# Performance work log

Measured on AMD Instinct MI355X. Metric: run time of the kernel, lower is better.

The kernel has to match this reference:

```python
import jax, jax.numpy as jnp
import numpy as np

B, T, H, LATENT, P = 64, 256, 1024, 256, 128


def _lstm_layer(x, h0, c0, Wih, Whh, bih, bhh):
    """PyTorch-convention single-direction LSTM layer.
    x: (B,T,Din); returns hidden sequence (B,T,H). Gate order: i,f,g,o."""
    # Precompute the input contribution for all timesteps in one big GEMM.
    xg = jnp.einsum('btd,gd->btg', x, Wih) + bih + bhh  # (B,T,4H)

    def step(carry, xg_t):
        h, c = carry
        gates = xg_t + h @ Whh.T  # (B,4H)
        i, f, g, o = jnp.split(gates, 4, axis=-1)
        c = jax.nn.sigmoid(f) * c + jax.nn.sigmoid(i) * jnp.tanh(g)
        h = jax.nn.sigmoid(o) * jnp.tanh(c)
        return (h, c), h

    (_, _), hs = jax.lax.scan(step, (h0, c0), jnp.swapaxes(xg, 0, 1))
    return jnp.swapaxes(hs, 0, 1)  # (B,T,H)


def setup_inputs() -> dict:
    key = jax.random.key(0)
    ks = jax.random.split(key, 8)
    s = lambda fan_in: 1.0 / np.sqrt(fan_in)
    return {
        'z': jax.random.normal(ks[0], (B, LATENT), jnp.float32),
        'target_seq': jax.random.uniform(ks[1], (B, T, P), jnp.float32),
        'fc_init_w': jax.random.normal(ks[2], (H, LATENT), jnp.float32) * s(LATENT),
        'fc_init_b': jnp.zeros((H,), jnp.float32),
        'start_token': jax.random.normal(ks[3], (1, 1, P), jnp.float32) * 0.1,
        'W_ih_l0': jax.random.normal(ks[4], (4 * H, P), jnp.float32) * s(P),
        'W_hh_l0': jax.random.normal(ks[5], (4 * H, H), jnp.float32) * s(H),
        'b_ih_l0': jnp.zeros((4 * H,), jnp.float32),
        'b_hh_l0': jnp.zeros((4 * H,), jnp.float32),
        'W_ih_l1': jax.random.normal(ks[6], (4 * H, H), jnp.float32) * s(H),
        'W_hh_l1': jax.random.normal(ks[7], (4 * H, H), jnp.float32) * s(H),
        'b_ih_l1': jnp.zeros((4 * H,), jnp.float32),
        'b_hh_l1': jnp.zeros((4 * H,), jnp.float32),
        'out_w': jax.random.normal(jax.random.fold_in(key, 99), (P, H), jnp.float32) * s(H),
        'out_b': jnp.zeros((P,), jnp.float32),
    }


def reference(z, target_seq, fc_init_w, fc_init_b, start_token,
              W_ih_l0, W_hh_l0, b_ih_l0, b_hh_l0,
              W_ih_l1, W_hh_l1, b_ih_l1, b_hh_l1,
              out_w, out_b):
    # h0 = fc_init(z), shared across both LSTM layers (repeat over num_layers).
    h0 = z @ fc_init_w.T + fc_init_b  # (B,H)
    c0 = jnp.zeros_like(h0)
    # Full teacher forcing (teacher_forcing_ratio=1.0): input at step t is
    # target_seq[:, t-1]; step 0 uses the learned start token. Dropout is in
    # eval mode (identity).
    x_in = jnp.concatenate(
        [jnp.broadcast_to(start_token, (z.shape[0], 1, start_token.shape[-1])),
         target_seq[:, :-1, :]], axis=1)  # (B,T,P)
    h1 = _lstm_layer(x_in, h0, c0, W_ih_l0, W_hh_l0, b_ih_l0, b_hh_l0)
    h2 = _lstm_layer(h1, h0, c0, W_ih_l1, W_hh_l1, b_ih_l1, b_hh_l1)
    return jax.nn.sigmoid(jnp.einsum('bth,ph->btp', h2, out_w) + out_b)  # (B,T,P)
```

## Files before the change

### kernel.cpp

```cpp
#include <hip/hip_runtime.h>
#include <hip/hip_bf16.h>
#include <stdint.h>

typedef __attribute__((ext_vector_type(8))) short short8;
typedef __attribute__((ext_vector_type(4))) float floatx4;

#define B_ 64
#define T_ 256
#define H_ 1024
#define LATENT_ 256
#define P_ 128
#define BH_ (B_ * H_)
#define MFMA_(a, b, c) __builtin_amdgcn_mfma_f32_16x16x32_bf16(a, b, c, 0, 0, 0)
#define PBI(n, row) (((n) + 4 * (row)) & 31)

#define PBUF_OFF 0
#define WHH_OFF  65536
#define WIH0_OFF 131072
#define LDS_TOTAL 139264

#define SLOTS 258
#define CIDX(lay, slot) (((size_t)(lay) * SLOTS + (slot)) * 256)
#define RIDX(lay, slot) (((size_t)(lay) * SLOTS + (slot)) * 128)
#define CNTW (2 * SLOTS * 256)
#define RDYW (2 * SLOTS * 128)


__device__ __forceinline__ float sigmoidf_(float x) {
    return 1.0f / (1.0f + __expf(-x));
}
__device__ __forceinline__ float tanh_fast(float x) {
    float e = __expf(2.0f * x);
    return 1.0f - 2.0f / (e + 1.0f);
}

__global__ __launch_bounds__(256) void cvt_f2b(
    const float* __restrict__ src, __hip_bfloat16* __restrict__ dst, int n)
{
    int i = (blockIdx.x * 256 + threadIdx.x) * 4;
    if (i < n) {
        float4 v = *(const float4*)(src + i);
        dst[i + 0] = __float2bfloat16(v.x);
        dst[i + 1] = __float2bfloat16(v.y);
        dst[i + 2] = __float2bfloat16(v.z);
        dst[i + 3] = __float2bfloat16(v.w);
    }
}

__global__ __launch_bounds__(256) void h0_kernel(
    const float* __restrict__ z,
    const float* __restrict__ fw,
    const float* __restrict__ fb,
    __hip_bfloat16* __restrict__ h1dst,
    __hip_bfloat16* __restrict__ h2dst,
    unsigned* __restrict__ cnt,
    unsigned* __restrict__ rdy)
{
    int idx = blockIdx.x * 256 + threadIdx.x;
    for (int i = idx; i < CNTW; i += 65536) cnt[i] = 0u;
    for (int i = idx; i < RDYW; i += 65536) {
        int slot = (i >> 7) % SLOTS;
        rdy[i] = (slot == 0) ? 1u : 0u;
    }
    int b = idx >> 10, j = idx & 1023;
    const float* zp = z + b * LATENT_;
    const float* wp = fw + j * LATENT_;
    float acc = fb[j];
    for (int k = 0; k < LATENT_; k += 4) {
        float4 zv = *(const float4*)(zp + k);
        float4 wv = *(const float4*)(wp + k);
        acc += zv.x * wv.x + zv.y * wv.y + zv.z * wv.z + zv.w * wv.w;
    }
    __hip_bfloat16 hb = __float2bfloat16(acc);
    int off = ((j >> 3) * 64 + b) * 8 + (j & 7);
    h1dst[off] = hb;
    h2dst[off] = hb;
}

struct PParams {
    const __hip_bfloat16 *tseqb, *stokb;
    const __hip_bfloat16 *Wih0b, *Whh0b, *Wih1b, *Whh1b, *owb;
    const float *bih0, *bhh0, *bih1, *bhh1, *ob;
    __hip_bfloat16 *h1seq;
    __hip_bfloat16 *h2seq;
    float* out;
    unsigned* cnt;
    unsigned* rdy;
};

__global__ __launch_bounds__(512, 2) void lstm_persistent(PParams p)
{
    extern __shared__ char dynlds[];
    float (*pbuf)[64][32] = (float (*)[64][32])(dynlds + PBUF_OFF);
    short8* whh8 = (short8*)(dynlds + WHH_OFF);
    short8* wx8  = (short8*)(dynlds + WIH0_OFF);

    const int tid  = threadIdx.x;
    const int bid  = blockIdx.x;
    const int wv   = tid >> 6;
    const int l    = tid & 63;
    const int l15  = l & 15;
    const int quad = l >> 4;
    const int ks   = quad * 8;
    const bool isL1 = bid < 128;
    const int colbase = (isL1 ? bid : bid - 128) * 8;
    const int hblk = colbase >> 3;
    const int r0l  = (l15 >> 3) * 8 + (l15 & 7);
    const int row0 = ((l15 >> 3)    ) * H_ + colbase + (l15 & 7);
    const int row1 = ((l15 >> 3) + 2) * H_ + colbase + (l15 & 7);

    auto h1slot = [&](int t) { return p.h1seq + (size_t)(t + 1) * BH_; };
    auto h2slot = [&](int t) { return p.h2seq + (size_t)(t + 1) * BH_; };

    auto wspin = [&](int lay, int slot) {
        if (l == 0) {
            const unsigned* rf = p.rdy + RIDX(lay, slot) + wv * 16;
            while (__hip_atomic_load(rf, __ATOMIC_RELAXED,
                                     __HIP_MEMORY_SCOPE_AGENT) == 0u)
                __builtin_amdgcn_s_sleep(2);
        }
        asm volatile("" ::: "memory");
    };

    {
        const short* Wh = (const short*)(isL1 ? p.Whh1b : p.Whh0b);
        for (int i = tid; i < 32 * 128; i += 512) {
            int r = i >> 7, kc = i & 127;
            int grow = (r >> 3) * H_ + colbase + (r & 7);
            whh8[r * 128 + (kc ^ (r & 7))] =
                *(const short8*)(Wh + (size_t)grow * H_ + kc * 8);
        }
        if (!isL1) {
            const short* Wx = (const short*)p.Wih0b;
            for (int i = tid; i < 32 * 16; i += 512) {
                int r = i >> 4, kc = i & 15;
                int grow = (r >> 3) * H_ + colbase + (r & 7);
                wx8[r * 16 + (kc ^ (r & 7))] =
                    *(const short8*)(Wx + (size_t)grow * P_ + kc * 8);
            }
        }
    }
    __syncthreads();

    const int cm  = tid >> 3;
    const int c0  = tid & 7;
    const int cj0 = colbase + c0;
    const float* bi = isL1 ? p.bih1 : p.bih0;
    const float* bh = isL1 ? p.bhh1 : p.bhh0;
    float bs[4];
#pragma unroll
    for (int g = 0; g < 4; ++g)
        bs[g] = bi[g * H_ + cj0] + bh[g * H_ + cj0];
    float creg = 0.0f;

    const int lay = isL1 ? 1 : 0;

    for (int phase = 0; phase <= T_; ++phase) {
        const bool doGemm = isL1 ? (phase >= 1) : (phase < T_);
        const int t = isL1 ? phase - 1 : phase;
        if (!doGemm) continue;

        floatx4 acc[8] = {};
        if (isL1) {
            wspin(1, phase - 1);
            const short* A2 = (const short*)h2slot(t - 1);
            short8 af2[16];
#pragma unroll
            for (int c = 0; c < 4; ++c)
#pragma unroll
                for (int mt = 0; mt < 4; ++mt) {
                    int kR = wv * 16 + c * 4 + quad;
                    af2[c * 4 + mt] = *(const short8*)(A2 +
                        ((long)(kR * 64 + mt * 16 + l15) << 3));
                }
            wspin(0, phase);
            const short* A1 = (const short*)h1slot(t);
            short8 af1[16];
#pragma unroll
            for (int c = 0; c < 4; ++c)
#pragma unroll
                for (int mt = 0; mt < 4; ++mt) {
                    int kR = wv * 16 + c * 4 + quad;
                    af1[c * 4 + mt] = *(const short8*)(A1 +
                        ((long)(kR * 64 + mt * 16 + l15) << 3));
                }
#pragma unroll
            for (int c = 0; c < 4; ++c) {
                int kR = wv * 16 + c * 4 + quad;
                short8 b0 = whh8[r0l * 128 + (kR ^ (r0l & 7))];
                short8 b1 = whh8[(r0l + 16) * 128 + (kR ^ (r0l & 7))];
#pragma unroll
                for (int mt = 0; mt < 4; ++mt) {
                    acc[2 * mt]     = MFMA_(af2[c * 4 + mt], b0, acc[2 * mt]);
                    acc[2 * mt + 1] = MFMA_(af2[c * 4 + mt], b1, acc[2 * mt + 1]);
                }
            }
            const short* w0 = (const short*)p.Wih1b + (long)row0 * H_;
            const short* w1 = (const short*)p.Wih1b + (long)row1 * H_;
#pragma unroll
            for (int c = 0; c < 4; ++c) {
                int kR = wv * 16 + c * 4 + quad;
                short8 b0 = *(const short8*)(w0 + kR * 8);
                short8 b1 = *(const short8*)(w1 + kR * 8);
#pragma unroll
                for (int mt = 0; mt < 4; ++mt) {
                    acc[2 * mt]     = MFMA_(af1[c * 4 + mt], b0, acc[2 * mt]);
                    acc[2 * mt + 1] = MFMA_(af1[c * 4 + mt], b1, acc[2 * mt + 1]);
                }
            }
        } else {
            const short* Ax; long xstr;
            if (t == 0) { Ax = (const short*)p.stokb; xstr = 0; }
            else { Ax = (const short*)p.tseqb + (long)(t - 1) * P_; xstr = (long)T_ * P_; }
            short8 xf[4];
            if (wv < 4) {
#pragma unroll
                for (int mt = 0; mt < 4; ++mt)
                    xf[mt] = *(const short8*)(Ax + (long)(mt * 16 + l15) * xstr + wv * 32 + ks);
            }
            wspin(0, phase);
            const short* Ah = (const short*)h1slot(t - 1);
            short8 af[16];
#pragma unroll
            for (int c = 0; c < 4; ++c)
#pragma unroll
                for (int mt = 0; mt < 4; ++mt) {
                    int kR = wv * 16 + c * 4 + quad;
                    af[c * 4 + mt] = *(const short8*)(Ah +
                        ((long)(kR * 64 + mt * 16 + l15) << 3));
                }
            if (wv < 4) {
                int kcx = wv * 4 + quad;
                short8 b0 = wx8[r0l * 16 + (kcx ^ (r0l & 7))];
                short8 b1 = wx8[(r0l + 16) * 16 + (kcx ^ (r0l & 7))];
#pragma unroll
                for (int mt = 0; mt < 4; ++mt) {
                    acc[2 * mt]     = MFMA_(xf[mt], b0, acc[2 * mt]);
                    acc[2 * mt + 1] = MFMA_(xf[mt], b1, acc[2 * mt + 1]);
                }
            }
#pragma unroll
            for (int c = 0; c < 4; ++c) {
                int kR = wv * 16 + c * 4 + quad;
                short8 b0 = whh8[r0l * 128 + (kR ^ (r0l & 7))];
                short8 b1 = whh8[(r0l + 16) * 128 + (kR ^ (r0l & 7))];
#pragma unroll
                for (int mt = 0; mt < 4; ++mt) {
                    acc[2 * mt]     = MFMA_(af[c * 4 + mt], b0, acc[2 * mt]);
                    acc[2 * mt + 1] = MFMA_(af[c * 4 + mt], b1, acc[2 * mt + 1]);
                }
            }
        }
#pragma unroll
        for (int mt = 0; mt < 4; ++mt)
#pragma unroll
            for (int nt = 0; nt < 2; ++nt)
#pragma unroll
                for (int r = 0; r < 4; ++r) {
                    int row = mt * 16 + quad * 4 + r;
                    pbuf[wv][row][PBI(nt * 16 + l15, row)] = acc[2 * mt + nt][r];
                }
        __syncthreads();

        {
            float v[4];
#pragma unroll
            for (int g = 0; g < 4; ++g) v[g] = bs[g];
#pragma unroll
            for (int w2 = 0; w2 < 8; ++w2)
#pragma unroll
                for (int g = 0; g < 4; ++g)
                    v[g] += pbuf[w2][cm][PBI(8 * g + c0, cm)];
            float cn = sigmoidf_(v[1]) * creg + sigmoidf_(v[0]) * tanh_fast(v[2]);
            float hv = sigmoidf_(v[3]) * tanh_fast(cn);
            creg = cn;
            __hip_bfloat16* hdst = isL1 ? h2slot(t) : h1slot(t);
            __hip_bfloat16 hb = __float2bfloat16(hv);
            unsigned short hu = *(unsigned short*)&hb;
            __hip_atomic_store((unsigned short*)hdst + hblk * 512 + tid, hu,
                               __ATOMIC_RELAXED, __HIP_MEMORY_SCOPE_AGENT);
        }

        __syncthreads();
        if (tid == 0) {
            __hip_atomic_fetch_add(p.cnt + CIDX(lay, t + 1) + (hblk >> 3) * 16,
                                   1u, __ATOMIC_RELAXED, __HIP_MEMORY_SCOPE_AGENT);
            if (bid == 128 || bid == 0) {
                unsigned* cb = p.cnt + CIDX(lay, t + 1);
                for (;;) {
                    unsigned ok = 1;
#pragma unroll
                    for (int i2 = 0; i2 < 16; ++i2)
                        ok &= (__hip_atomic_load(cb + i2 * 16, __ATOMIC_RELAXED,
                                                 __HIP_MEMORY_SCOPE_AGENT) >= 8u);
                    if (ok) break;
                    __builtin_amdgcn_s_sleep(1);
                }
                asm volatile("" ::: "memory");
                unsigned* rb = p.rdy + RIDX(lay, t + 1);
#pragma unroll
                for (int w = 0; w < 8; ++w)
                    __hip_atomic_store(rb + w * 16, 1u,
                                       __ATOMIC_RELAXED, __HIP_MEMORY_SCOPE_AGENT);
            }
        }
        __syncthreads();
    }

    {
        const int t = bid;
        wspin(1, t + 1);
        __syncthreads();

        const int nh = wv >> 1, kh = wv & 1;
        const short* A  = (const short*)h2slot(t);
        const short* Wb = (const short*)p.owb;
        floatx4 oacc[8] = {};
        for (int c = 0; c < 16; ++c) {
            int kk = kh * 512 + c * 32 + ks;
            short8 b0 = *(const short8*)(Wb + (long)(nh * 32 + l15) * H_ + kk);
            short8 b1 = *(const short8*)(Wb + (long)(nh * 32 + 16 + l15) * H_ + kk);
#pragma unroll
            for (int mt = 0; mt < 4; ++mt) {
                short8 a = *(const short8*)(A +
                    ((long)((kh * 64 + c * 4 + quad) * 64 + mt * 16 + l15) << 3));
                oacc[2 * mt]     = MFMA_(a, b0, oacc[2 * mt]);
                oacc[2 * mt + 1] = MFMA_(a, b1, oacc[2 * mt + 1]);
            }
        }
#pragma unroll
        for (int mt = 0; mt < 4; ++mt)
#pragma unroll
            for (int nt = 0; nt < 2; ++nt)
#pragma unroll
                for (int r = 0; r < 4; ++r) {
                    int row = mt * 16 + quad * 4 + r;
                    pbuf[wv][row][PBI(nt * 16 + l15, row)] = oacc[2 * mt + nt][r];
                }
        __syncthreads();
        for (int i = tid; i < 64 * 128; i += 512) {
            int m = i >> 7, pp2 = i & 127;
            int nh2 = pp2 >> 5, pc = pp2 & 31;
            float v = pbuf[2 * nh2][m][PBI(pc, m)] + pbuf[2 * nh2 + 1][m][PBI(pc, m)]
                    + p.ob[pp2];
            p.out[(long)m * (T_ * P_) + (long)t * P_ + pp2] = sigmoidf_(v);
        }
    }
}

extern "C" void kernel_launch(void* const* d_in, const int* in_sizes, int n_in,
                              void* d_out, int out_size, void* d_ws, size_t ws_size,
                              hipStream_t stream) {
    const float* z    = (const float*)d_in[0];
    const float* tseq = (const float*)d_in[1];
    const float* fw   = (const float*)d_in[2];
    const float* fb   = (const float*)d_in[3];
    const float* stok = (const float*)d_in[4];
    const float* Wih0 = (const float*)d_in[5];
    const float* Whh0 = (const float*)d_in[6];
    const float* bih0 = (const float*)d_in[7];
    const float* bhh0 = (const float*)d_in[8];
    const float* Wih1 = (const float*)d_in[9];
    const float* Whh1 = (const float*)d_in[10];
    const float* bih1 = (const float*)d_in[11];
    const float* bhh1 = (const float*)d_in[12];
    const float* ow   = (const float*)d_in[13];
    const float* ob   = (const float*)d_in[14];
    float* out = (float*)d_out;

    const size_t FULLH = (size_t)(T_ + 1) * BH_ * 2;
    char* ws = (char*)d_ws;
    size_t off = 0;
    __hip_bfloat16* Wih0b = (__hip_bfloat16*)(ws + off); off += (size_t)4 * H_ * P_ * 2;
    __hip_bfloat16* Whh0b = (__hip_bfloat16*)(ws + off); off += (size_t)4 * H_ * H_ * 2;
    __hip_bfloat16* Wih1b = (__hip_bfloat16*)(ws + off); off += (size_t)4 * H_ * H_ * 2;
    __hip_bfloat16* Whh1b = (__hip_bfloat16*)(ws + off); off += (size_t)4 * H_ * H_ * 2;
    __hip_bfloat16* owb   = (__hip_bfloat16*)(ws + off); off += (size_t)P_ * H_ * 2;
    __hip_bfloat16* tseqb = (__hip_bfloat16*)(ws + off); off += (size_t)B_ * T_ * P_ * 2;
    __hip_bfloat16* stokb = (__hip_bfloat16*)(ws + off); off += 256;
    __hip_bfloat16* h1seq = (__hip_bfloat16*)(ws + off); off += FULLH;
    __hip_bfloat16* h2seq = (__hip_bfloat16*)(ws + off); off += FULLH;
    unsigned* cnt         = (unsigned*)(ws + off);       off += (size_t)CNTW * 4;
    unsigned* rdy         = (unsigned*)(ws + off);       off += (size_t)RDYW * 4;

    auto cvt = [&](const float* s, __hip_bfloat16* d, int n) {
        hipLaunchKernelGGL(cvt_f2b, dim3((n / 4 + 255) / 256), dim3(256), 0, stream, s, d, n);
    };
    cvt(Wih0, Wih0b, 4 * H_ * P_);
    cvt(Whh0, Whh0b, 4 * H_ * H_);
    cvt(Wih1, Wih1b, 4 * H_ * H_);
    cvt(Whh1, Whh1b, 4 * H_ * H_);
    cvt(ow,   owb,   P_ * H_);
    cvt(tseq, tseqb, B_ * T_ * P_);
    cvt(stok, stokb, P_);

    hipLaunchKernelGGL(h0_kernel, dim3(256), dim3(256), 0, stream,
                       z, fw, fb, h1seq, h2seq, cnt, rdy);

    PParams pp;
    pp.tseqb = tseqb; pp.stokb = stokb;
    pp.Wih0b = Wih0b; pp.Whh0b = Whh0b; pp.Wih1b = Wih1b; pp.Whh1b = Whh1b;
    pp.owb = owb;
    pp.bih0 = bih0; pp.bhh0 = bhh0; pp.bih1 = bih1; pp.bhh1 = bhh1; pp.ob = ob;
    pp.h1seq = h1seq; pp.h2seq = h2seq;
    pp.out = out;
    pp.cnt = cnt; pp.rdy = rdy;

    hipFuncSetAttribute((const void*)lstm_persistent,
                        hipFuncAttributeMaxDynamicSharedMemorySize, LDS_TOTAL);
    void* args[] = { &pp };
    hipLaunchCooperativeKernel((void*)lstm_persistent, dim3(256), dim3(512),
                               args, LDS_TOTAL, stream);
}
```

Baseline: 1.922 ms.

## Replace two-level counter/ready-flag barrier with per-group counters polled directly

Drops the aggregator blocks that waited on all per-step counters and then set ready flags. Each block now increments one of 8 group counters per layer and step, and consumers poll only the group counter covering the hidden-state slice their wave needs, waiting for 16 arrivals. This removes one hop of cross-block signalling and the trailing __syncthreads from the recurrent critical path. In exchange each wave waits only on its own slice, so correctness relies on the wave-to-group mapping matching the data each wave reads.

New measurement: 2.628 ms. +36.8%, slower.

```diff
diff --git a/kernel.cpp b/kernel.cpp
--- a/kernel.cpp
+++ b/kernel.cpp
@@ -20,10 +20,8 @@
 #define LDS_TOTAL 139264
 
 #define SLOTS 258
-#define CIDX(lay, slot) (((size_t)(lay) * SLOTS + (slot)) * 256)
-#define RIDX(lay, slot) (((size_t)(lay) * SLOTS + (slot)) * 128)
-#define CNTW (2 * SLOTS * 256)
-#define RDYW (2 * SLOTS * 128)
+#define CLINE(lay, slot, g) (((((size_t)(lay) * SLOTS + (slot)) << 3) + (g)) << 4)
+#define CNTW (2 * SLOTS * 8 * 16)
 
 
 __device__ __forceinline__ float sigmoidf_(float x) {
@@ -53,14 +51,13 @@
     const float* __restrict__ fb,
     __hip_bfloat16* __restrict__ h1dst,
     __hip_bfloat16* __restrict__ h2dst,
-    unsigned* __restrict__ cnt,
-    unsigned* __restrict__ rdy)
+    unsigned* __restrict__ cnt)
 {
     int idx = blockIdx.x * 256 + threadIdx.x;
-    for (int i = idx; i < CNTW; i += 65536) cnt[i] = 0u;
-    for (int i = idx; i < RDYW; i += 65536) {
-        int slot = (i >> 7) % SLOTS;
-        rdy[i] = (slot == 0) ? 1u : 0u;
+    for (int i = idx; i < CNTW; i += 65536) {
+        int line = i >> 4;
+        int slot = (line >> 3) % SLOTS;
+        cnt[i] = ((i & 15) == 0 && slot == 0) ? 16u : 0u;
     }
     int b = idx >> 10, j = idx & 1023;
     const float* zp = z + b * LATENT_;
@@ -85,7 +82,6 @@
     __hip_bfloat16 *h2seq;
     float* out;
     unsigned* cnt;
-    unsigned* rdy;
 };
 
 __global__ __launch_bounds__(512, 2) void lstm_persistent(PParams p)
@@ -114,9 +110,9 @@
 
     auto wspin = [&](int lay, int slot) {
         if (l == 0) {
-            const unsigned* rf = p.rdy + RIDX(lay, slot) + wv * 16;
-            while (__hip_atomic_load(rf, __ATOMIC_RELAXED,
-                                     __HIP_MEMORY_SCOPE_AGENT) == 0u)
+            const unsigned* cf = p.cnt + CLINE(lay, slot, wv);
+            while (__hip_atomic_load(cf, __ATOMIC_RELAXED,
+                                     __HIP_MEMORY_SCOPE_AGENT) < 16u)
                 __builtin_amdgcn_s_sleep(2);
         }
         asm volatile("" ::: "memory");
@@ -154,6 +150,7 @@
     float creg = 0.0f;
 
     const int lay = isL1 ? 1 : 0;
+    const int agrp = hblk >> 4;
 
     for (int phase = 0; phase <= T_; ++phase) {
         const bool doGemm = isL1 ? (phase >= 1) : (phase < T_);
@@ -282,34 +279,22 @@
         }
 
         __syncthreads();
-        if (tid == 0) {
-            __hip_atomic_fetch_add(p.cnt + CIDX(lay, t + 1) + (hblk >> 3) * 16,
-                                   1u, __ATOMIC_RELAXED, __HIP_MEMORY_SCOPE_AGENT);
-            if (bid == 128 || bid == 0) {
-                unsigned* cb = p.cnt + CIDX(lay, t + 1);
-                for (;;) {
-                    unsigned ok = 1;
-#pragma unroll
-                    for (int i2 = 0; i2 < 16; ++i2)
-                        ok &= (__hip_atomic_load(cb + i2 * 16, __ATOMIC_RELAXED,
-                                                 __HIP_MEMORY_SCOPE_AGENT) >= 8u);
-                    if (ok) break;
-                    __builtin_amdgcn_s_sleep(1);
-                }
-                asm volatile("" ::: "memory");
-                unsigned* rb = p.rdy + RIDX(lay, t + 1);
-#pragma unroll
-                for (int w = 0; w < 8; ++w)
-                    __hip_atomic_store(rb + w * 16, 1u,
-                                       __ATOMIC_RELAXED, __HIP_MEMORY_SCOPE_AGENT);
-            }
-        }
-        __syncthreads();
+        if (tid == 0)
+            __hip_atomic_fetch_add(p.cnt + CLINE(lay, t + 1, agrp), 1u,
+                                   __ATOMIC_RELAXED, __HIP_MEMORY_SCOPE_AGENT);
     }
 
     {
         const int t = bid;
-        wspin(1, t + 1);
+        if (tid == 0) {
+            for (int g = 0; g < 8; ++g) {
+                const unsigned* cf = p.cnt + CLINE(1, t + 1, g);
+                while (__hip_atomic_load(cf, __ATOMIC_RELAXED,
+                                         __HIP_MEMORY_SCOPE_AGENT) < 16u)
+                    __builtin_amdgcn_s_sleep(2);
+            }
+        }
+        asm volatile("" ::: "memory");
         __syncthreads();
 
         const int nh = wv >> 1, kh = wv & 1;
@@ -381,7 +366,6 @@
     __hip_bfloat16* h1seq = (__hip_bfloat16*)(ws + off); off += FULLH;
     __hip_bfloat16* h2seq = (__hip_bfloat16*)(ws + off); off += FULLH;
     unsigned* cnt         = (unsigned*)(ws + off);       off += (size_t)CNTW * 4;
-    unsigned* rdy         = (unsigned*)(ws + off);       off += (size_t)RDYW * 4;
 
     auto cvt = [&](const float* s, __hip_bfloat16* d, int n) {
         hipLaunchKernelGGL(cvt_f2b, dim3((n / 4 + 255) / 256), dim3(256), 0, stream, s, d, n);
@@ -395,7 +379,7 @@
     cvt(stok, stokb, P_);
 
     hipLaunchKernelGGL(h0_kernel, dim3(256), dim3(256), 0, stream,
-                       z, fw, fb, h1seq, h2seq, cnt, rdy);
+                       z, fw, fb, h1seq, h2seq, cnt);
 
     PParams pp;
     pp.tseqb = tseqb; pp.stokb = stokb;
@@ -404,7 +388,7 @@
     pp.bih0 = bih0; pp.bhh0 = bhh0; pp.bih1 = bih1; pp.bhh1 = bhh1; pp.ob = ob;
     pp.h1seq = h1seq; pp.h2seq = h2seq;
     pp.out = out;
-    pp.cnt = cnt; pp.rdy = rdy;
+    pp.cnt = cnt;
 
     hipFuncSetAttribute((const void*)lstm_persistent,
                         hipFuncAttributeMaxDynamicSharedMemorySize, LDS_TOTAL);
```
